# Kernel tuning notes

Measured on AMD Instinct MI355X. Metric: run time of the kernel, lower is better.

Reference implementation:

```python
import jax, jax.numpy as jnp
import numpy as np

D, H, N, T, B = 32, 128, 128, 256, 64   # input_dim, n_units, N_units, time_depth, batch
HEADS, THR, SHORT = 4, 0.01, 2
HD = H // HEADS


def setup_inputs() -> dict:
    key = jax.random.key(0)
    ks = iter(jax.random.split(key, 64))
    rn = lambda *s: jax.random.normal(next(ks), s, dtype=jnp.float32) * 0.1
    inp = {"x": jax.random.normal(next(ks), (B, T, D), dtype=jnp.float32)}
    for n_ in ["U_j", "U_i", "U_f", "U_o"]:
        inp[n_] = rn(D, 1, H)
    for n_ in ["W_j", "W_i", "W_f", "W_o"]:
        inp[n_] = rn(D, H, H)
    for n_ in ["B_j", "B_i", "B_f", "B_o"]:
        inp[n_] = jnp.full((D, H), 0.01, dtype=jnp.float32)
    for n_ in ["u_j", "u_i", "u_f", "u_o"]:
        inp[n_] = rn(D, N)
    for n_ in ["w_j", "w_i", "w_f", "w_o"]:
        inp[n_] = rn(N, N)
    for n_ in ["b_j", "b_i", "b_f", "b_o"]:
        inp[n_] = jnp.full((N,), 0.01, dtype=jnp.float32)
    inp["qkv_w"] = rn(3 * H, H)      # nn.Linear(H, 3H, bias=False) weight
    inp["out_w"] = rn(H, H)          # attn out_proj weight
    inp["h_proj_w"] = rn(N, H)       # nn.Linear(H, N, bias=False) weight
    inp["w_p"] = rn(N, 1)
    inp["b_p"] = jnp.zeros((1,), dtype=jnp.float32)
    return inp


def reference(x, U_j, U_i, U_f, U_o, W_j, W_i, W_f, W_o, B_j, B_i, B_f, B_o,
              u_j, u_i, u_f, u_o, w_j, w_i, w_f, w_o, b_j, b_i, b_f, b_o,
              qkv_w, out_w, h_proj_w, w_p, b_p):
    scale = 1.0 / jnp.sqrt(jnp.asarray(HD, dtype=x.dtype))

    def attention(h):  # h: (B, D, H) -> (B, D, H) cross-variable MHA
        qkv = h @ qkv_w.T                              # (B, D, 3H)
        q, k, v = jnp.split(qkv, 3, axis=-1)
        rs = lambda a: a.reshape(h.shape[0], D, HEADS, HD).transpose(0, 2, 1, 3)
        q, k, v = rs(q), rs(k), rs(v)                  # (B, heads, D, HD)
        scores = jnp.einsum('bhid,bhjd->bhij', q, k) * scale
        a = jax.nn.softmax(scores, axis=-1)
        a = jnp.where(a >= THR, a, jnp.zeros_like(a))
        ctx = jnp.einsum('bhij,bhjd->bhid', a, v)      # (B, heads, D, HD)
        ctx = ctx.transpose(0, 2, 1, 3).reshape(h.shape[0], D, H)
        return ctx @ out_w.T

    # per-variable input contributions: x_t[:, :, None] * U[:, 0, :]
    Uj, Ui, Uf, Uo = U_j[:, 0, :], U_i[:, 0, :], U_f[:, 0, :], U_o[:, 0, :]

    def step(carry, inputs):
        t, x_t = inputs                                # x_t: (B, D)
        h_var, c_var, h_mix, c_mix = carry
        xu = x_t[:, :, None]                            # (B, D, 1)
        j_var = jnp.tanh(jnp.einsum('bij,ijk->bik', h_var, W_j) + xu * Uj + B_j)
        i_var = jax.nn.sigmoid(jnp.einsum('bij,ijk->bik', h_var, W_i) + xu * Ui + B_i)
        f_var = jax.nn.sigmoid(jnp.einsum('bij,ijk->bik', h_var, W_f) + xu * Uf + B_f)
        o_var = jax.nn.sigmoid(jnp.einsum('bij,ijk->bik', h_var, W_o) + xu * Uo + B_o)
        c_var = c_var * f_var + i_var * j_var
        h_var = o_var * jnp.tanh(c_var)

        i_t = jax.nn.sigmoid(x_t @ u_i + h_mix @ w_i + b_i)
        f_t = jax.nn.sigmoid(x_t @ u_f + h_mix @ w_f + b_f)
        o_t = jax.nn.sigmoid(x_t @ u_o + h_mix @ w_o + b_o)
        j_t = jnp.tanh(x_t @ u_j + h_mix @ w_j + b_j)
        c_mix = f_t * c_mix + i_t * j_t
        h_mix_lstm = o_t * jnp.tanh(c_mix)

        z = attention(h_var)
        h_hat = z.mean(axis=1) @ h_proj_w.T            # (B, N)
        pred = h_hat @ w_p + b_p                       # (B, 1)
        h_mix = jnp.where(t > SHORT, h_hat, h_mix_lstm)
        return (h_var, c_var, h_mix, c_mix), pred

    z32 = jnp.zeros((x.shape[0], D, H), dtype=x.dtype)
    carry0 = (z32, z32,
              jnp.zeros((x.shape[0], N), dtype=x.dtype),
              jnp.zeros((x.shape[0], N), dtype=x.dtype))
    ts = jnp.arange(T - 1)
    xs = x.transpose(1, 0, 2)[: T - 1]                 # (T-1, B, D)
    _, preds = jax.lax.scan(step, carry0, (ts, xs))    # (T-1, B, 1)
    pred = preds[SHORT + 1:].transpose(1, 0, 2)        # (B, T-SHORT-2, 1)
    return pred
```

## Files before the change

### kernel.cpp

```cpp
#include <hip/hip_runtime.h>
#include <hip/hip_bf16.h>

typedef __hip_bfloat16 bf16;
typedef _Float16 f16x2 __attribute__((ext_vector_type(2)));
typedef _Float16 half8 __attribute__((ext_vector_type(8)));
typedef float f32x4 __attribute__((ext_vector_type(4)));

#define D_ 32
#define H_ 128
#define T_ 256
#define B_ 64
#define NSTEP 255
#define NOUT 252

#define F32_PROBE 0x3C23D70Au

#define MFMA_F16(A, B, C) __builtin_amdgcn_mfma_f32_16x16x32_f16(A, B, C, 0, 0, 0)

__device__ __forceinline__ float sigm(float v) {
    return __builtin_amdgcn_rcpf(1.0f + __expf(-v));
}
__device__ __forceinline__ float tanh_f(float x) {
    float xc = fminf(fmaxf(x, -9.0f), 9.0f);
    float e = __expf(-2.0f * xc);
    return (1.0f - e) * __builtin_amdgcn_rcpf(1.0f + e);
}

__device__ __forceinline__ unsigned int packh2(float a, float b) {
    union { unsigned int u; f16x2 h; } c;
    c.h[0] = (_Float16)a; c.h[1] = (_Float16)b;
    return c.u;
}
union U4H8 { uint4 u; half8 h; };
__device__ __forceinline__ half8 as_h8(uint4 u) { U4H8 x; x.u = u; return x.h; }

struct CvtArgs {
    const void* src[18];
    float* dst[18];
    int cnt[18];
    const unsigned int* probe;
};

__global__ __launch_bounds__(256) void k_convert(CvtArgs a)
{
    const bool isf32 = (*a.probe == F32_PROBE);
    const int seg = blockIdx.y;
    const int n = a.cnt[seg];
    const void* s = a.src[seg];
    float* dgt = a.dst[seg];
    for (int i = blockIdx.x * 256 + threadIdx.x; i < n; i += gridDim.x * 256) {
        float v;
        if (isf32) v = ((const float*)s)[i];
        else       v = __uint_as_float(((unsigned int)((const unsigned short*)s)[i]) << 16);
        dgt[i] = v;
    }
}

__global__ __launch_bounds__(256) void k_xpose(const float* __restrict__ xf,
                                              float* __restrict__ xT)
{
    __shared__ float tile[64][33];
    const int t = blockIdx.x;
    const int tid = threadIdx.x;
    for (int idx = tid; idx < 2048; idx += 256) {
        int b = idx >> 5, dd = idx & 31;
        tile[b][dd] = xf[((size_t)b * T_ + t) * D_ + dd];
    }
    __syncthreads();
    for (int idx = tid; idx < 2048; idx += 256) {
        int dd = idx >> 6, b = idx & 63;
        xT[((size_t)dd * T_ + t) * B_ + b] = tile[b][dd];
    }
}

__global__ __launch_bounds__(256) void k_pack(const float* __restrict__ qw,
                                              unsigned int* __restrict__ wpk)
{
    int idx = blockIdx.x * 256 + threadIdx.x;
    int k2 = idx & 63, row = idx >> 6;
    wpk[idx] = packh2(qw[row * 128 + 2 * k2], qw[row * 128 + 2 * k2 + 1]);
}

__global__ __launch_bounds__(1024, 1) void k_recur(
    const float* __restrict__ xT, const float* __restrict__ wf,
    const float* __restrict__ uf, const float* __restrict__ bfv,
    float* __restrict__ cstg, unsigned int* __restrict__ h2g,
    unsigned int* __restrict__ hbw,
    int t0, int t1, int slots)
{
    __shared__ __align__(16) unsigned int hsw[2][512];
    __shared__ float xs[2048];

    const int tid  = threadIdx.x;
    const int lane = tid & 63;
    const int w    = tid >> 6;
    const int bx   = blockIdx.x;
    const int d    = bx >> 3;
    const int b0   = (bx & 7) * 8;
    const int l15  = lane & 15;
    const int l4   = lane >> 4;
    const int bb   = l15 & 7;
    const int sel  = l15 >> 3;

    const int ntot = (t1 - t0) * 8;
    for (int idx = tid; idx < ntot; idx += 1024) {
        int tr = idx >> 3, bbx = idx & 7;
        xs[idx] = xT[((size_t)d * T_ + (t0 + tr)) * B_ + b0 + bbx];
    }

    uint4 wfr[2][4];
    #pragma unroll
    for (int mtl = 0; mtl < 2; ++mtl) {
        const int c = w * 32 + mtl * 16 + l15;
        const int g = c & 3, h = c >> 2;
        const float* Wp = wf + (((size_t)g * 32 + d) * 128) * 128 + h;
        #pragma unroll
        for (int ks = 0; ks < 4; ++ks) {
            const int jb = ks * 32 + l4 * 8;
            uint4 u;
            u.x = packh2(Wp[(jb + 0) * 128], Wp[(jb + 1) * 128]);
            u.y = packh2(Wp[(jb + 2) * 128], Wp[(jb + 3) * 128]);
            u.z = packh2(Wp[(jb + 4) * 128], Wp[(jb + 5) * 128]);
            u.w = packh2(Wp[(jb + 6) * 128], Wp[(jb + 7) * 128]);
            wfr[mtl][ks] = u;
        }
    }
    float ur[2][4], br[2][4];
    #pragma unroll
    for (int mtl = 0; mtl < 2; ++mtl) {
        const int hq = w * 8 + mtl * 4 + l4;
        #pragma unroll
        for (int g = 0; g < 4; ++g) {
            ur[mtl][g] = uf [g * 4096 + d * H_ + hq];
            br[mtl][g] = bfv[g * 4096 + d * H_ + hq];
        }
    }

    float cs0;
    if (t0 == 0) cs0 = 0.f;
    else         cs0 = cstg[bx * 1024 + tid];

    {
        unsigned int* tgt = hsw[t0 & 1];
        if (t0 == 0) { if (tid < 512) tgt[tid] = 0u; }
        else         { if (tid < 512) tgt[tid] = h2g[bx * 512 + tid]; }
    }
    __syncthreads();

    const int m = w * 4 + sel * 2 + (l4 >> 1);
    const bool writer = !(l4 & 1);
    unsigned int pend = 0u;

    for (int t = t0; t < t1; ++t) {
        if (t > t0 && writer) {
            const int tp = t - 1;
            if (tp >= 3) {
                const int slotp = (tp - 3) % slots;
                hbw[(((size_t)slotp * B_ + b0 + bb) * D_ + d) * 64 + m] = pend;
            }
        }

        const unsigned int* hr = hsw[t & 1];
        unsigned int* hw       = hsw[(t & 1) ^ 1];

        uint4 hb[4];
        #pragma unroll
        for (int ks = 0; ks < 4; ++ks) {
            const int jc = ks * 4 + l4;
            hb[ks] = *(const uint4*)&hr[bb * 64 + (((jc ^ bb) & 15) << 2)];
        }
        const float xb = xs[(t - t0) * 8 + bb];

        f32x4 acc[2];
        #pragma unroll
        for (int mtl = 0; mtl < 2; ++mtl) {
            f32x4 a;
            a[0] = xb * ur[mtl][0] + br[mtl][0];
            a[1] = xb * ur[mtl][1] + br[mtl][1];
            a[2] = xb * ur[mtl][2] + br[mtl][2];
            a[3] = xb * ur[mtl][3] + br[mtl][3];
            acc[mtl] = a;
        }
        #pragma unroll
        for (int ks = 0; ks < 4; ++ks) {
            #pragma unroll
            for (int mtl = 0; mtl < 2; ++mtl)
                acc[mtl] = MFMA_F16(as_h8(wfr[mtl][ks]), as_h8(hb[ks]), acc[mtl]);
        }

        float a0 = sel ? acc[1][0] : acc[0][0];
        float a1 = sel ? acc[1][1] : acc[0][1];
        float a2 = sel ? acc[1][2] : acc[0][2];
        float a3 = sel ? acc[1][3] : acc[0][3];
        float jj = tanh_f(a0);
        float ii = sigm(a1);
        float ff = sigm(a2);
        float oo = sigm(a3);
        float cn = cs0 * ff + ii * jj;
        cs0 = cn;
        float hv = oo * tanh_f(cn);
        float pv = __shfl_xor(hv, 16);
        if (writer) {
            unsigned int hp = packh2(hv, pv);
            hw[bb * 64 + (((w ^ bb) & 15) << 2) + (sel * 2 + (l4 >> 1))] = hp;
            pend = hp;
        }
        __syncthreads();
    }

    {
        const int tp = t1 - 1;
        if (tp >= 3 && writer) {
            const int slotp = (tp - 3) % slots;
            hbw[(((size_t)slotp * B_ + b0 + bb) * D_ + d) * 64 + m] = pend;
        }
    }

    {
        const unsigned int* fin = hsw[t1 & 1];
        if (tid < 512) h2g[bx * 512 + tid] = fin[tid];
        cstg[bx * 1024 + tid] = cs0;
    }
}

#define QK_OFF  0
#define VT_OFF  16384
#define A_OFF   0
#define RED_OFF 24576
#define ATT_LDS 24608

__global__ __launch_bounds__(256, 2) void k_attn(
    const unsigned int* __restrict__ hbuf, const unsigned int* __restrict__ wpk,
    const float* __restrict__ vc, const unsigned int* __restrict__ probe,
    void* __restrict__ outv, int t0, int slots, int nt)
{
    __shared__ __align__(16) char S[ATT_LDS];

    const int tid  = threadIdx.x;
    const int lane = tid & 63;
    const int w    = tid >> 6;
    const int b    = blockIdx.y;
    const int tbase = t0 + 2 * blockIdx.x;
    const int ntt  = (nt - 2 * (int)blockIdx.x >= 2) ? 2 : 1;
    const int l15  = lane & 15;
    const int l4   = lane >> 4;

    uint4 wfr[6][4];
    #pragma unroll
    for (int mi = 0; mi < 6; ++mi) {
        const int mt = w + 4 * mi;
        const int r  = mt * 16 + l15;
        #pragma unroll
        for (int ks = 0; ks < 4; ++ks)
            wfr[mi][ks] = ((const uint4*)wpk)[r * 16 + ks * 4 + l4];
    }
    const float vcr0 = vc[w * 32 + l15];
    const float vcr1 = vc[w * 32 + 16 + l15];

    for (int tt = 0; tt < ntt; ++tt) {
        if (tt) __syncthreads();

        const int t = tbase + tt;
        const int slot = (t - 3) % slots;
        const uint4* hsrc4 =
            (const uint4*)(hbuf + ((size_t)slot * B_ + b) * (D_ * 64));
        uint4 hfr[2][4];
        #pragma unroll
        for (int nt_ = 0; nt_ < 2; ++nt_) {
            const int dd = nt_ * 16 + l15;
            #pragma unroll
            for (int ks = 0; ks < 4; ++ks)
                hfr[nt_][ks] = hsrc4[dd * 16 + ks * 4 + l4];
        }
        #pragma unroll
        for (int mi = 0; mi < 6; ++mi) {
            const int mt  = w + 4 * mi;
            const int r0  = mt * 16 + (l4 << 2);
            const int tau = r0 >> 7;
            const int hd2 = (r0 >> 5) & 3;
            const int d0  = r0 & 31;
            #pragma unroll
            for (int nt_ = 0; nt_ < 2; ++nt_) {
                f32x4 acc = {0.f, 0.f, 0.f, 0.f};
                #pragma unroll
                for (int ks = 0; ks < 4; ++ks)
                    acc = MFMA_F16(as_h8(wfr[mi][ks]), as_h8(hfr[nt_][ks]), acc);
                const int ddc = nt_ * 16 + l15;
                if (tau < 2) {
                    unsigned int u0 = packh2(acc[0], acc[1]);
                    unsigned int u1 = packh2(acc[2], acc[3]);
                    const int c = (d0 >> 3) ^ ((ddc >> 1) & 3);
                    *(uint2*)(S + QK_OFF + (tau * 4 + hd2) * 2048 + ddc * 64
                              + c * 16 + ((2 * d0) & 15)) = make_uint2(u0, u1);
                } else {
                    #pragma unroll
                    for (int q = 0; q < 4; ++q) {
                        const int j = d0 + q;
                        const int c = (ddc >> 3) ^ ((j >> 1) & 3);
                        *(_Float16*)(S + VT_OFF + hd2 * 2048 + j * 64
                                     + c * 16 + ((2 * ddc) & 15)) = (_Float16)acc[q];
                    }
                }
            }
        }
        __syncthreads();

        uint4 qa[2], ka[2];
        #pragma unroll
        for (int It = 0; It < 2; ++It) {
            const int dd = It * 16 + l15;
            const int c = l4 ^ ((dd >> 1) & 3);
            qa[It] = *(const uint4*)(S + QK_OFF + (0 * 4 + w) * 2048 + dd * 64 + c * 16);
            ka[It] = *(const uint4*)(S + QK_OFF + (1 * 4 + w) * 2048 + dd * 64 + c * 16);
        }
        f32x4 st[2][2];
        #pragma unroll
        for (int Et = 0; Et < 2; ++Et)
            #pragma unroll
            for (int It = 0; It < 2; ++It) {
                f32x4 z = {0.f, 0.f, 0.f, 0.f};
                st[Et][It] = MFMA_F16(as_h8(ka[Et]), as_h8(qa[It]), z);
            }
        const float scale = 0.17677669529663687f;
        float mx[2], sum[2];
        #pragma unroll
        for (int It = 0; It < 2; ++It) {
            float m = -1e30f;
            #pragma unroll
            for (int Et = 0; Et < 2; ++Et)
                #pragma unroll
                for (int q = 0; q < 4; ++q) {
                    st[Et][It][q] *= scale;
                    m = fmaxf(m, st[Et][It][q]);
                }
            m = fmaxf(m, __shfl_xor(m, 16));
            m = fmaxf(m, __shfl_xor(m, 32));
            mx[It] = m;
        }
        #pragma unroll
        for (int It = 0; It < 2; ++It) {
            float s = 0.f;
            #pragma unroll
            for (int Et = 0; Et < 2; ++Et)
                #pragma unroll
                for (int q = 0; q < 4; ++q) {
                    float e = __expf(st[Et][It][q] - mx[It]);
                    st[Et][It][q] = e;
                    s += e;
                }
            s += __shfl_xor(s, 16);
            s += __shfl_xor(s, 32);
            sum[It] = s;
        }
        const float inv0 = 1.0f / sum[0];
        const float inv1 = 1.0f / sum[1];
        #pragma unroll
        for (int It = 0; It < 2; ++It) {
            const int i = It * 16 + l15;
            const float inv = It ? inv1 : inv0;
            #pragma unroll
            for (int Et = 0; Et < 2; ++Et)
                #pragma unroll
                for (int q = 0; q < 4; ++q) {
                    float a = st[Et][It][q] * inv;
                    if (a < 0.01f) a = 0.f;
                    const int e = Et * 16 + (l4 << 2) + q;
                    const int c = (e >> 3) ^ ((i >> 1) & 3);
                    *(_Float16*)(S + A_OFF + w * 2048 + i * 64
                                 + c * 16 + ((2 * e) & 15)) = (_Float16)a;
                }
        }
        uint4 aa[2], vb[2];
        #pragma unroll
        for (int It = 0; It < 2; ++It) {
            const int i = It * 16 + l15;
            const int c = l4 ^ ((i >> 1) & 3);
            aa[It] = *(const uint4*)(S + A_OFF + w * 2048 + i * 64 + c * 16);
        }
        #pragma unroll
        for (int Jt = 0; Jt < 2; ++Jt) {
            const int j = Jt * 16 + l15;
            const int c = l4 ^ ((j >> 1) & 3);
            vb[Jt] = *(const uint4*)(S + VT_OFF + w * 2048 + j * 64 + c * 16);
        }
        f32x4 ct[2][2];
        #pragma unroll
        for (int It = 0; It < 2; ++It)
            #pragma unroll
            for (int Jt = 0; Jt < 2; ++Jt) {
                f32x4 z = {0.f, 0.f, 0.f, 0.f};
                ct[It][Jt] = MFMA_F16(as_h8(aa[It]), as_h8(vb[Jt]), z);
            }
        float p = 0.f;
        #pragma unroll
        for (int Jt = 0; Jt < 2; ++Jt) {
            float cs_ = 0.f;
            #pragma unroll
            for (int It = 0; It < 2; ++It)
                #pragma unroll
                for (int q = 0; q < 4; ++q) cs_ += ct[It][Jt][q];
            cs_ += __shfl_xor(cs_, 16);
            cs_ += __shfl_xor(cs_, 32);
            p += cs_ * (Jt ? vcr1 : vcr0);
        }
        p *= (1.0f / 32.0f);
        p += __shfl_xor(p, 1);
        p += __shfl_xor(p, 2);
        p += __shfl_xor(p, 4);
        p += __shfl_xor(p, 8);
        if (lane == 0)
            *(float*)(S + RED_OFF + (tt * 4 + w) * 4) = p;
    }
    __syncthreads();

    if (tid < ntt) {
        const float* rd = (const float*)(S + RED_OFF);
        float r = rd[tid * 4] + rd[tid * 4 + 1] + rd[tid * 4 + 2] + rd[tid * 4 + 3]
                + vc[128];
        const int t = tbase + tid;
        size_t oidx = (size_t)b * NOUT + (t - 3);
        if (*probe == F32_PROBE) ((float*)outv)[oidx] = r;
        else                     ((bf16*)outv)[oidx]  = __float2bfloat16(r);
    }
}

__global__ __launch_bounds__(128) void k_vcomb(
    const float* __restrict__ hprj, const float* __restrict__ outw,
    const float* __restrict__ wp, const float* __restrict__ bp,
    float* __restrict__ vc)
{
    __shared__ float tmp[128];
    int j = threadIdx.x;
    float s = 0.f;
    for (int n = 0; n < 128; ++n) s += hprj[n * 128 + j] * wp[n];
    tmp[j] = s;
    __syncthreads();
    float v = 0.f;
    for (int c = 0; c < 128; ++c) v += outw[c * 128 + j] * tmp[c];
    vc[j] = v;
    if (j == 0) vc[128] = bp[0];
}

extern "C" void kernel_launch(void* const* d_in, const int* in_sizes, int n_in,
                              void* d_out, int out_size, void* d_ws, size_t ws_size,
                              hipStream_t stream)
{
    float* ws = (float*)d_ws;
    float* xf    = ws;
    float* cstg  = ws;
    unsigned int* h2g = (unsigned int*)(ws + 262144);
    float* xT    = ws + 524288;
    float* wf    = ws + 1048576;
    float* uf    = ws + 3145728;
    float* bfv   = ws + 3162112;
    float* qkvwf = ws + 3178496;
    float* outwf = ws + 3227648;
    float* hprjf = ws + 3244032;
    float* wpf   = ws + 3260416;
    float* bpf   = ws + 3260544;
    float* vcomb = ws + 3260608;
    unsigned int* wpk = (unsigned int*)(ws + 3260800);
    unsigned short* hbuf = (unsigned short*)((char*)d_ws + 13141504);

    const unsigned int* probe = (const unsigned int*)d_in[9];

    CvtArgs ca;
    ca.src[0] = d_in[0];  ca.dst[0] = xf;  ca.cnt[0] = B_ * T_ * D_;
    for (int g = 0; g < 4; ++g) {
        ca.src[1 + g] = d_in[5 + g]; ca.dst[1 + g] = wf + (size_t)g * 524288; ca.cnt[1 + g] = 524288;
        ca.src[5 + g] = d_in[1 + g]; ca.dst[5 + g] = uf + g * 4096;           ca.cnt[5 + g] = 4096;
        ca.src[9 + g] = d_in[9 + g]; ca.dst[9 + g] = bfv + g * 4096;          ca.cnt[9 + g] = 4096;
    }
    ca.src[13] = d_in[25]; ca.dst[13] = qkvwf; ca.cnt[13] = 49152;
    ca.src[14] = d_in[26]; ca.dst[14] = outwf; ca.cnt[14] = 16384;
    ca.src[15] = d_in[27]; ca.dst[15] = hprjf; ca.cnt[15] = 16384;
    ca.src[16] = d_in[28]; ca.dst[16] = wpf;   ca.cnt[16] = 128;
    ca.src[17] = d_in[29]; ca.dst[17] = bpf;   ca.cnt[17] = 1;
    ca.probe = probe;

    k_convert<<<dim3(64, 18), dim3(256), 0, stream>>>(ca);
    k_xpose<<<dim3(T_), dim3(256), 0, stream>>>(xf, xT);
    k_pack<<<dim3(96), dim3(256), 0, stream>>>(qkvwf, wpk);
    k_vcomb<<<dim3(1), dim3(128), 0, stream>>>(hprjf, outwf, wpf, bpf, vcomb);

    long avail = (long)ws_size - 13141504L;
    int cap = (avail > 0) ? (int)(avail / 524288L) : 0;
    if (cap > NOUT) cap = NOUT;
    if (cap < 1) cap = 1;

    int t0c = 0;
    while (t0c < NSTEP) {
        int prod0 = (t0c < 3) ? 3 : t0c;
        int t1c = prod0 + cap;
        if (t1c > NSTEP) t1c = NSTEP;
        int nt = t1c - prod0;
        k_recur<<<dim3(256), dim3(1024), 0, stream>>>(
            xT, wf, uf, bfv, cstg, h2g, (unsigned int*)hbuf, t0c, t1c, cap);
        k_attn<<<dim3((nt + 1) / 2, 64), dim3(256), 0, stream>>>(
            (const unsigned int*)hbuf, wpk, vcomb, probe, d_out, prod0, cap, nt);
        t0c = t1c;
    }
}
```

Before: 522.3 us.

## Coalesce h-buffer and packed QKV weight layouts; process four timesteps per attention block

```diff
diff --git a/kernel.cpp b/kernel.cpp
--- a/kernel.cpp
+++ b/kernel.cpp
@@ -77,8 +77,15 @@
                                               unsigned int* __restrict__ wpk)
 {
     int idx = blockIdx.x * 256 + threadIdx.x;
-    int k2 = idx & 63, row = idx >> 6;
-    wpk[idx] = packh2(qw[row * 128 + 2 * k2], qw[row * 128 + 2 * k2 + 1]);
+    int e   = idx & 3;
+    int w4  = idx >> 2;
+    int l15 = w4 & 15;
+    int l4  = (w4 >> 4) & 3;
+    int ks  = (w4 >> 6) & 3;
+    int mt  = w4 >> 8;
+    int r   = mt * 16 + l15;
+    int k2  = (ks * 4 + l4) * 4 + e;
+    wpk[idx] = packh2(qw[r * 128 + 2 * k2], qw[r * 128 + 2 * k2 + 1]);
 }
 
 __global__ __launch_bounds__(1024, 1) void k_recur(
@@ -147,7 +154,7 @@
     }
     __syncthreads();
 
-    const int m = w * 4 + sel * 2 + (l4 >> 1);
+    const int wrd = sel * 2 + (l4 >> 1);
     const bool writer = !(l4 & 1);
     unsigned int pend = 0u;
 
@@ -156,7 +163,7 @@
             const int tp = t - 1;
             if (tp >= 3) {
                 const int slotp = (tp - 3) % slots;
-                hbw[(((size_t)slotp * B_ + b0 + bb) * D_ + d) * 64 + m] = pend;
+                hbw[((((size_t)slotp * B_ + b0 + bb) * 16 + w) * 32 + d) * 4 + wrd] = pend;
             }
         }
 
@@ -202,7 +209,7 @@
         float pv = __shfl_xor(hv, 16);
         if (writer) {
             unsigned int hp = packh2(hv, pv);
-            hw[bb * 64 + (((w ^ bb) & 15) << 2) + (sel * 2 + (l4 >> 1))] = hp;
+            hw[bb * 64 + (((w ^ bb) & 15) << 2) + wrd] = hp;
             pend = hp;
         }
         __syncthreads();
@@ -212,7 +219,7 @@
         const int tp = t1 - 1;
         if (tp >= 3 && writer) {
             const int slotp = (tp - 3) % slots;
-            hbw[(((size_t)slotp * B_ + b0 + bb) * D_ + d) * 64 + m] = pend;
+            hbw[((((size_t)slotp * B_ + b0 + bb) * 16 + w) * 32 + d) * 4 + wrd] = pend;
         }
     }
 
@@ -227,7 +234,8 @@
 #define VT_OFF  16384
 #define A_OFF   0
 #define RED_OFF 24576
-#define ATT_LDS 24608
+#define ATT_LDS 24640
+#define TT_     4
 
 __global__ __launch_bounds__(256, 2) void k_attn(
     const unsigned int* __restrict__ hbuf, const unsigned int* __restrict__ wpk,
@@ -240,19 +248,18 @@
     const int lane = tid & 63;
     const int w    = tid >> 6;
     const int b    = blockIdx.y;
-    const int tbase = t0 + 2 * blockIdx.x;
-    const int ntt  = (nt - 2 * (int)blockIdx.x >= 2) ? 2 : 1;
+    const int tbase = t0 + TT_ * blockIdx.x;
+    int ntt = nt - TT_ * (int)blockIdx.x;
+    if (ntt > TT_) ntt = TT_;
     const int l15  = lane & 15;
     const int l4   = lane >> 4;
 
     uint4 wfr[6][4];
     #pragma unroll
     for (int mi = 0; mi < 6; ++mi) {
-        const int mt = w + 4 * mi;
-        const int r  = mt * 16 + l15;
         #pragma unroll
         for (int ks = 0; ks < 4; ++ks)
-            wfr[mi][ks] = ((const uint4*)wpk)[r * 16 + ks * 4 + l4];
+            wfr[mi][ks] = ((const uint4*)wpk)[((w + 4 * mi) * 4 + ks) * 64 + lane];
     }
     const float vcr0 = vc[w * 32 + l15];
     const float vcr1 = vc[w * 32 + 16 + l15];
@@ -263,14 +270,13 @@
         const int t = tbase + tt;
         const int slot = (t - 3) % slots;
         const uint4* hsrc4 =
-            (const uint4*)(hbuf + ((size_t)slot * B_ + b) * (D_ * 64));
+            (const uint4*)hbuf + ((size_t)slot * B_ + b) * 512;
         uint4 hfr[2][4];
         #pragma unroll
         for (int nt_ = 0; nt_ < 2; ++nt_) {
-            const int dd = nt_ * 16 + l15;
             #pragma unroll
             for (int ks = 0; ks < 4; ++ks)
-                hfr[nt_][ks] = hsrc4[dd * 16 + ks * 4 + l4];
+                hfr[nt_][ks] = hsrc4[(ks * 4 + l4) * 32 + nt_ * 16 + l15];
         }
         #pragma unroll
         for (int mi = 0; mi < 6; ++mi) {
@@ -496,7 +502,7 @@
         int nt = t1c - prod0;
         k_recur<<<dim3(256), dim3(1024), 0, stream>>>(
             xT, wf, uf, bfv, cstg, h2g, (unsigned int*)hbuf, t0c, t1c, cap);
-        k_attn<<<dim3((nt + 1) / 2, 64), dim3(256), 0, stream>>>(
+        k_attn<<<dim3((nt + TT_ - 1) / TT_, 64), dim3(256), 0, stream>>>(
             (const unsigned int*)hbuf, wpk, vcomb, probe, d_out, prod0, cap, nt);
         t0c = t1c;
     }
```

Result: faster. 449.3 us (-14.0%).
